# Kernel tuning notes

Hardware: AMD Instinct MI355X
Metric: run time of the kernel (lower is better)

Reference implementation:

```python
import jax, jax.numpy as jnp
import numpy as np

HIDDEN = 128
VOCAB = 100000
NUM_CLASSES = 5
N_LEAVES = 65536  # complete binary tree -> 2*N_LEAVES-1 = 131071 nodes


def setup_inputs() -> dict:
    key = jax.random.key(0)
    ks = jax.random.split(key, 24)
    H, C = HIDDEN, NUM_CLASSES

    def w(k, o, i):
        return (jax.random.normal(k, (o, i), jnp.float32) / np.sqrt(i)).astype(jnp.float32)

    def b(k, o):
        return jax.random.normal(k, (o,), jnp.float32) * 0.01

    inp = {
        "leaf_tokens": jax.random.randint(ks[0], (N_LEAVES,), 0, VOCAB, dtype=jnp.int64 if jax.config.jax_enable_x64 else jnp.int32).astype(jnp.int32),
        "node_labels": jax.random.randint(ks[1], (2 * N_LEAVES - 1,), 0, NUM_CLASSES).astype(jnp.int32),
        "embed": jax.random.uniform(ks[2], (VOCAB, H), jnp.float32, -0.5 / H, 0.5 / H),
        "W_i_w": w(ks[3], H, H), "W_i_b": b(ks[4], H),
        "W_o_w": w(ks[5], H, H), "W_o_b": b(ks[6], H),
        "W_u_w": w(ks[7], H, H), "W_u_b": b(ks[8], H),
        "U_i_w": w(ks[9], H, 2 * H), "U_i_b": b(ks[10], H),
        "U_o_w": w(ks[11], H, 2 * H), "U_o_b": b(ks[12], H),
        "U_u_w": w(ks[13], H, 2 * H), "U_u_b": b(ks[14], H),
        "F1_w": w(ks[15], H, H), "F1_b": b(ks[16], H),
        "F2_w": w(ks[17], H, H), "F2_b": b(ks[18], H),
        "out_w": w(ks[19], C, H), "out_b": b(ks[20], C),
    }
    return inp


def reference(leaf_tokens, node_labels, embed,
              W_i_w, W_i_b, W_o_w, W_o_b, W_u_w, W_u_b,
              U_i_w, U_i_b, U_o_w, U_o_b, U_u_w, U_u_b,
              F1_w, F1_b, F2_w, F2_b, out_w, out_b):
    def aff(x, wgt, bias):
        return x @ wgt.T + bias

    # ---- leaves: x = embed[token]; c = sigmoid(W_i x) * tanh(W_u x) ----
    x = embed[leaf_tokens]                          # [L, H]
    i = jax.nn.sigmoid(aff(x, W_i_w, W_i_b))
    o = jax.nn.sigmoid(aff(x, W_o_w, W_o_b))
    u = jnp.tanh(aff(x, W_u_w, W_u_b))
    c = i * u
    h = o * jnp.tanh(c)
    outs = [aff(h, out_w, out_b)]                   # dropout is identity at eval

    # ---- internal levels, bottom-up, all same-depth nodes batched ----
    n_levels = int(np.log2(N_LEAVES))
    for _ in range(n_levels):
        hl, hr = h[0::2], h[1::2]                   # [n/2, H] each
        cl, cr = c[0::2], c[1::2]
        xc = jnp.concatenate([hl, hr], axis=1)      # [n/2, 2H]
        i = jax.nn.sigmoid(aff(xc, U_i_w, U_i_b))
        o = jax.nn.sigmoid(aff(xc, U_o_w, U_o_b))
        u = jnp.tanh(aff(xc, U_u_w, U_u_b))
        f1 = jax.nn.sigmoid(aff(hl, F1_w, F1_b))
        f2 = jax.nn.sigmoid(aff(hr, F2_w, F2_b))
        c = i * u + f1 * cl + f2 * cr
        h = o * jnp.tanh(c)
        outs.append(aff(h, out_w, out_b))

    outputs = jnp.concatenate(outs, axis=0)         # [2L-1, num_classes]
    return outputs, node_labels
```

## Files before the change

### kernel.cpp

```cpp
#include <hip/hip_runtime.h>
#include <hip/hip_bf16.h>
#include <math.h>

#define H    128
#define NC   5
#define LPI  264
#define LPL  136
#define HPAD 136
#define CBP  132

typedef unsigned short ushort_t;
using frag_ab = __attribute__((ext_vector_type(8))) short;
using frag_cd = __attribute__((ext_vector_type(4))) float;

__device__ __forceinline__ float fsig(float x) { return 1.0f / (1.0f + __expf(-x)); }
__device__ __forceinline__ float ftanh_(float x) {
    float e = __expf(-2.0f * fabsf(x));
    float t = (1.0f - e) / (1.0f + e);
    return copysignf(t, x);
}
__device__ __forceinline__ ushort_t f2bf(float f) {
    __hip_bfloat16 b = __float2bfloat16(f);
    return *reinterpret_cast<ushort_t*>(&b);
}

__global__ __launch_bounds__(256) void prep_weights(
    const float* __restrict__ Ui, const float* __restrict__ Uo, const float* __restrict__ Uu,
    const float* __restrict__ F1, const float* __restrict__ F2,
    const float* __restrict__ Wi, const float* __restrict__ Wo, const float* __restrict__ Wu,
    const float* __restrict__ Wout,
    ushort_t* __restrict__ Wf, ushort_t* __restrict__ Wlf, ushort_t* __restrict__ Woutf)
{
    int e = blockIdx.x * 256 + threadIdx.x;
    if (e < 131072) {
        int kc = e >> 12, rem = e & 4095;
        int n = rem >> 3, j7 = rem & 7;
        int k = kc * 8 + j7;
        int g = n >> 7, jc = n & 127;
        float v;
        if (g == 0)      v = Ui[jc * 256 + k];
        else if (g == 1) v = Uo[jc * 256 + k];
        else if (g == 2) v = Uu[jc * 256 + k];
        else             v = (k < 128) ? F1[jc * 128 + k] : F2[jc * 128 + k - 128];
        Wf[e] = f2bf(v);
    } else if (e < 180224) {
        int e2 = e - 131072;
        int kc = e2 / 3072, rem = e2 % 3072;
        int n = rem >> 3, j7 = rem & 7;
        int k = kc * 8 + j7;
        int g = n >> 7, jc = n & 127;
        float v = (g == 0) ? Wi[jc * 128 + k] : (g == 1) ? Wo[jc * 128 + k] : Wu[jc * 128 + k];
        Wlf[e2] = f2bf(v);
    } else {
        int e3 = e - 180224;
        int kcq = e3 >> 7, rem = e3 & 127;
        int col = rem >> 3, j7 = rem & 7;
        int k = kcq * 8 + j7;
        float v = (col < NC) ? Wout[col * H + k] : 0.0f;
        Woutf[e3] = f2bf(v);
    }
}

__global__ __launch_bounds__(512) void leaf_l1_mfma(
    const int* __restrict__ tokens, const float* __restrict__ embed,
    const ushort_t* __restrict__ Wlf, const ushort_t* __restrict__ Wf,
    const ushort_t* __restrict__ Woutf,
    const float* __restrict__ bi, const float* __restrict__ bo, const float* __restrict__ bu,
    const float* __restrict__ bui, const float* __restrict__ buo, const float* __restrict__ buu,
    const float* __restrict__ bf1, const float* __restrict__ bf2,
    const float* __restrict__ bout,
    const int* __restrict__ labels, float* __restrict__ lab_out,
    ushort_t* __restrict__ h1_out, float* __restrict__ c1_out,
    float* __restrict__ out_leaf, float* __restrict__ out_l1)
{
    __shared__ ushort_t xs [32 * LPL];
    __shared__ ushort_t hh [32 * HPAD];
    __shared__ float    cbL[32 * CBP];
    __shared__ ushort_t xs2[16 * LPI];
    const int tid = threadIdx.x;
    const int node_base  = blockIdx.x * 32;
    const int node1_base = blockIdx.x * 16;

    if (tid < 64) {
        int id = blockIdx.x * 64 + tid;
        if (id < 131071) lab_out[id] = (float)labels[id];
    }

    {
        int m = tid >> 4, kp = (tid & 15) * 8;
        const float* src = embed + (size_t)tokens[node_base + m] * H + kp;
        ushort_t tmp[8];
#pragma unroll
        for (int v = 0; v < 2; ++v) {
            float4 f = *(const float4*)(src + v * 4);
            tmp[v * 4 + 0] = f2bf(f.x); tmp[v * 4 + 1] = f2bf(f.y);
            tmp[v * 4 + 2] = f2bf(f.z); tmp[v * 4 + 3] = f2bf(f.w);
        }
        *(uint4*)&xs[m * LPL + kp] = *(uint4*)tmp;
    }

    const int w = tid >> 6, lane = tid & 63;
    const int mA = lane & 15, q = lane >> 4, nlane = lane & 15;

    frag_ab wb[4];
#pragma unroll
    for (int kc8 = 0; kc8 < 4; ++kc8)
        wb[kc8] = *(const frag_ab*)&Woutf[(((kc8 * 4 + q) * 16) + nlane) * 8];
    float bout_l = (nlane < NC) ? bout[nlane] : 0.0f;

    const int jt = w;
    const int j = jt * 16 + nlane;
    __syncthreads();

    frag_ab a[2][4];
#pragma unroll
    for (int t = 0; t < 2; ++t)
#pragma unroll
        for (int kc8 = 0; kc8 < 4; ++kc8)
            a[t][kc8] = *(const frag_ab*)&xs[(t * 16 + mA) * LPL + (kc8 * 4 + q) * 8];

    {
        frag_cd acc[3][2];
#pragma unroll
        for (int g = 0; g < 3; ++g)
#pragma unroll
            for (int t = 0; t < 2; ++t) acc[g][t] = (frag_cd){0.f, 0.f, 0.f, 0.f};
#pragma unroll
        for (int kc8 = 0; kc8 < 4; ++kc8) {
            int kcq = kc8 * 4 + q;
            const ushort_t* wp = &Wlf[((size_t)kcq * 384 + jt * 16 + nlane) * 8];
#pragma unroll
            for (int g = 0; g < 3; ++g) {
                frag_ab b = *(const frag_ab*)(wp + (size_t)g * H * 8);
                acc[g][0] = __builtin_amdgcn_mfma_f32_16x16x32_bf16(a[0][kc8], b, acc[g][0], 0, 0, 0);
                acc[g][1] = __builtin_amdgcn_mfma_f32_16x16x32_bf16(a[1][kc8], b, acc[g][1], 0, 0, 0);
            }
        }
        float bi_ = bi[j], bo_ = bo[j], bu_ = bu[j];
#pragma unroll
        for (int t = 0; t < 2; ++t)
#pragma unroll
            for (int r = 0; r < 4; ++r) {
                int nloc = t * 16 + q * 4 + r;
                float i_ = fsig(acc[0][t][r] + bi_);
                float o_ = fsig(acc[1][t][r] + bo_);
                float u_ = ftanh_(acc[2][t][r] + bu_);
                float c_ = i_ * u_;
                float h_ = o_ * ftanh_(c_);
                cbL[nloc * CBP + j] = c_;
                ushort_t hb = f2bf(h_);
                hh[nloc * HPAD + j] = hb;
                xs2[(nloc >> 1) * LPI + (nloc & 1) * H + j] = hb;
            }
    }
    __syncthreads();

    frag_ab a1[8];
#pragma unroll
    for (int kc8 = 0; kc8 < 8; ++kc8)
        a1[kc8] = *(const frag_ab*)&xs2[mA * LPI + (kc8 * 4 + q) * 8];

    if (w < 2) {
        frag_cd ha = (frag_cd){0.f, 0.f, 0.f, 0.f};
#pragma unroll
        for (int kc8 = 0; kc8 < 4; ++kc8) {
            frag_ab av = *(const frag_ab*)&hh[(w * 16 + mA) * HPAD + (kc8 * 4 + q) * 8];
            ha = __builtin_amdgcn_mfma_f32_16x16x32_bf16(av, wb[kc8], ha, 0, 0, 0);
        }
        if (nlane < NC) {
#pragma unroll
            for (int r = 0; r < 4; ++r)
                out_leaf[(size_t)(node_base + w * 16 + q * 4 + r) * NC + nlane] = ha[r] + bout_l;
        }
    }
    __syncthreads();

    {
        frag_cd acc[5];
#pragma unroll
        for (int g = 0; g < 5; ++g) acc[g] = (frag_cd){0.f, 0.f, 0.f, 0.f};
#pragma unroll
        for (int kc8 = 0; kc8 < 8; ++kc8) {
            int kcq = kc8 * 4 + q;
            const ushort_t* wp = &Wf[((size_t)kcq * 512 + jt * 16 + nlane) * 8];
#pragma unroll
            for (int g = 0; g < 4; ++g) {
                frag_ab b = *(const frag_ab*)(wp + (size_t)g * H * 8);
                int gi = (g < 3) ? g : (kc8 < 4 ? 3 : 4);
                acc[gi] = __builtin_amdgcn_mfma_f32_16x16x32_bf16(a1[kc8], b, acc[gi], 0, 0, 0);
            }
        }
        float bi_ = bui[j], bo_ = buo[j], bu_ = buu[j], b1_ = bf1[j], b2_ = bf2[j];
#pragma unroll
        for (int r = 0; r < 4; ++r) {
            int nloc = q * 4 + r;
            int nd = node1_base + nloc;
            float i_  = fsig(acc[0][r] + bi_);
            float o_  = fsig(acc[1][r] + bo_);
            float u_  = ftanh_(acc[2][r] + bu_);
            float f1_ = fsig(acc[3][r] + b1_);
            float f2_ = fsig(acc[4][r] + b2_);
            float cl = cbL[(2 * nloc) * CBP + j];
            float cr = cbL[(2 * nloc + 1) * CBP + j];
            float c_ = fmaf(i_, u_, fmaf(f1_, cl, f2_ * cr));
            float h_ = o_ * ftanh_(c_);
            c1_out[(size_t)nd * H + j] = c_;
            ushort_t hb = f2bf(h_);
            h1_out[(size_t)nd * H + j] = hb;
            hh[nloc * HPAD + j] = hb;
        }
    }
    __syncthreads();

    if (w == 0) {
        frag_cd ha = (frag_cd){0.f, 0.f, 0.f, 0.f};
#pragma unroll
        for (int kc8 = 0; kc8 < 4; ++kc8) {
            frag_ab av = *(const frag_ab*)&hh[mA * HPAD + (kc8 * 4 + q) * 8];
            ha = __builtin_amdgcn_mfma_f32_16x16x32_bf16(av, wb[kc8], ha, 0, 0, 0);
        }
        if (nlane < NC) {
#pragma unroll
            for (int r = 0; r < 4; ++r)
                out_l1[(size_t)(node1_base + q * 4 + r) * NC + nlane] = ha[r] + bout_l;
        }
    }
}

__global__ __launch_bounds__(512) void subtree_mfma(
    const ushort_t* __restrict__ h_prev, const float* __restrict__ c_prev,
    const ushort_t* __restrict__ Wf, const ushort_t* __restrict__ Woutf,
    const float* __restrict__ bui, const float* __restrict__ buo, const float* __restrict__ buu,
    const float* __restrict__ bf1, const float* __restrict__ bf2,
    const float* __restrict__ bout,
    ushort_t* __restrict__ h_out, float* __restrict__ c_out,
    float* __restrict__ out_base)
{
    __shared__ ushort_t xsA[32 * LPI];
    __shared__ ushort_t xsB[16 * LPI];
    __shared__ float    cbA[32 * CBP];
    __shared__ float    cbB[16 * CBP];
    __shared__ ushort_t hh [32 * HPAD];
    const int tid = threadIdx.x;
    const int NB  = gridDim.x;

    {
        int m = tid >> 4, kp = (tid & 15) * 16;
        const uint4* s = (const uint4*)(h_prev +
            ((size_t)2 * (blockIdx.x * 32 + m) + (kp >> 7)) * H + (kp & 127));
        uint4* d = (uint4*)&xsA[m * LPI + kp];
        d[0] = s[0]; d[1] = s[1];
    }

    const int w = tid >> 6, lane = tid & 63;
    const int mA = lane & 15, q = lane >> 4, nlane = lane & 15;

    frag_ab wb[4];
#pragma unroll
    for (int kc8 = 0; kc8 < 4; ++kc8)
        wb[kc8] = *(const frag_ab*)&Woutf[(((kc8 * 4 + q) * 16) + nlane) * 8];
    float bout_l = (nlane < NC) ? bout[nlane] : 0.0f;

    const int jt = w;
    const int j = jt * 16 + nlane;
    const float bi_ = bui[j], bo_ = buo[j], bu_ = buu[j], b1_ = bf1[j], b2_ = bf2[j];

    size_t out_off = 0;
    for (int lev = 0; lev < 4; ++lev) {
        const int N = 32 >> lev;
        const int ntiles = (N + 15) >> 4;
        const int gbase = blockIdx.x * N;
        ushort_t* xs_cur = (lev & 1) ? xsB : xsA;
        ushort_t* xs_nxt = (lev & 1) ? xsA : xsB;
        float*    cb_out = (lev & 1) ? cbB : cbA;
        const float* cb_in = (lev & 1) ? cbA : cbB;
        __syncthreads();

        for (int t = 0; t < ntiles; ++t) {
            frag_cd acc[5];
#pragma unroll
            for (int g = 0; g < 5; ++g) acc[g] = (frag_cd){0.f, 0.f, 0.f, 0.f};
#pragma unroll
            for (int kc8 = 0; kc8 < 8; ++kc8) {
                int kcq = kc8 * 4 + q;
                frag_ab av = *(const frag_ab*)&xs_cur[(t * 16 + mA) * LPI + kcq * 8];
                const ushort_t* wp = &Wf[((size_t)kcq * 512 + jt * 16 + nlane) * 8];
#pragma unroll
                for (int g = 0; g < 4; ++g) {
                    frag_ab b = *(const frag_ab*)(wp + (size_t)g * H * 8);
                    int gi = (g < 3) ? g : (kc8 < 4 ? 3 : 4);
                    acc[gi] = __builtin_amdgcn_mfma_f32_16x16x32_bf16(av, b, acc[gi], 0, 0, 0);
                }
            }
#pragma unroll
            for (int r = 0; r < 4; ++r) {
                int nloc = t * 16 + q * 4 + r;
                if (nloc < N) {
                    float i_  = fsig(acc[0][r] + bi_);
                    float o_  = fsig(acc[1][r] + bo_);
                    float u_  = ftanh_(acc[2][r] + bu_);
                    float f1_ = fsig(acc[3][r] + b1_);
                    float f2_ = fsig(acc[4][r] + b2_);
                    float cl, cr;
                    if (lev == 0) {
                        cl = c_prev[((size_t)2 * (gbase + nloc)) * H + j];
                        cr = c_prev[((size_t)2 * (gbase + nloc) + 1) * H + j];
                    } else {
                        cl = cb_in[(2 * nloc) * CBP + j];
                        cr = cb_in[(2 * nloc + 1) * CBP + j];
                    }
                    float c_ = fmaf(i_, u_, fmaf(f1_, cl, f2_ * cr));
                    float h_ = o_ * ftanh_(c_);
                    ushort_t hb = f2bf(h_);
                    hh[nloc * HPAD + j] = hb;
                    if (lev < 3) {
                        cb_out[nloc * CBP + j] = c_;
                        xs_nxt[(nloc >> 1) * LPI + (nloc & 1) * H + j] = hb;
                    } else {
                        c_out[(size_t)(gbase + nloc) * H + j] = c_;
                        h_out[(size_t)(gbase + nloc) * H + j] = hb;
                    }
                }
            }
        }
        __syncthreads();
        if (w < ntiles) {
            frag_cd ha = (frag_cd){0.f, 0.f, 0.f, 0.f};
#pragma unroll
            for (int kc8 = 0; kc8 < 4; ++kc8) {
                frag_ab av = *(const frag_ab*)&hh[(w * 16 + mA) * HPAD + (kc8 * 4 + q) * 8];
                ha = __builtin_amdgcn_mfma_f32_16x16x32_bf16(av, wb[kc8], ha, 0, 0, 0);
            }
            if (nlane < NC) {
#pragma unroll
                for (int r = 0; r < 4; ++r) {
                    int nd = w * 16 + q * 4 + r;
                    if (nd < N)
                        out_base[out_off + (size_t)(gbase + nd) * NC + nlane] = ha[r] + bout_l;
                }
            }
        }
        out_off += (size_t)NB * N * NC;
    }
}

__global__ __launch_bounds__(512) void tail_mfma(
    const ushort_t* __restrict__ h_prev, const float* __restrict__ c_prev,
    const ushort_t* __restrict__ Wf, const ushort_t* __restrict__ Woutf,
    const float* __restrict__ bui, const float* __restrict__ buo, const float* __restrict__ buu,
    const float* __restrict__ bf1, const float* __restrict__ bf2,
    const float* __restrict__ bout, float* __restrict__ out)
{
    __shared__ ushort_t xsA[64 * LPI];
    __shared__ ushort_t xsB[32 * LPI];
    __shared__ float    cbA[64 * H];
    __shared__ float    cbB[32 * H];
    __shared__ ushort_t hh[64 * HPAD];
    const int tid = threadIdx.x;
    const int w = tid >> 6, lane = tid & 63;
    const int mA = lane & 15, q = lane >> 4, nlane = lane & 15;

    {
        int m = tid >> 3, kp = (tid & 7) * 32;
        const uint4* s = (const uint4*)(h_prev + ((size_t)2 * m + (kp >> 7)) * H + (kp & 127));
        uint4* d = (uint4*)&xsA[m * LPI + kp];
#pragma unroll
        for (int i = 0; i < 4; ++i) d[i] = s[i];
    }

    frag_ab wb[4];
#pragma unroll
    for (int kc8 = 0; kc8 < 4; ++kc8)
        wb[kc8] = *(const frag_ab*)&Woutf[(((kc8 * 4 + q) * 16) + nlane) * 8];
    float bout_l = (nlane < NC) ? bout[nlane] : 0.0f;

    const int jt = w;
    const int j = jt * 16 + nlane;
    const float bi_ = bui[j], bo_ = buo[j], bu_ = buu[j], b1_ = bf1[j], b2_ = bf2[j];

    float* outp = out;
    for (int lev = 0; lev < 7; ++lev) {
        const int N = 64 >> lev;
        const int ntiles = (N + 15) >> 4;
        ushort_t* xs_cur = (lev & 1) ? xsB : xsA;
        ushort_t* xs_nxt = (lev & 1) ? xsA : xsB;
        float*    cb_out = (lev & 1) ? cbB : cbA;
        const float* cb_in = (lev & 1) ? cbA : cbB;
        __syncthreads();

        for (int t = 0; t < ntiles; ++t) {
            frag_cd acc[5];
#pragma unroll
            for (int g = 0; g < 5; ++g) acc[g] = (frag_cd){0.f, 0.f, 0.f, 0.f};
#pragma unroll
            for (int kc8 = 0; kc8 < 8; ++kc8) {
                int kcq = kc8 * 4 + q;
                frag_ab av = *(const frag_ab*)&xs_cur[(t * 16 + mA) * LPI + kcq * 8];
                const ushort_t* wp = &Wf[((size_t)kcq * 512 + jt * 16 + nlane) * 8];
#pragma unroll
                for (int g = 0; g < 4; ++g) {
                    frag_ab b = *(const frag_ab*)(wp + (size_t)g * H * 8);
                    int gi = (g < 3) ? g : (kc8 < 4 ? 3 : 4);
                    acc[gi] = __builtin_amdgcn_mfma_f32_16x16x32_bf16(av, b, acc[gi], 0, 0, 0);
                }
            }
#pragma unroll
            for (int r = 0; r < 4; ++r) {
                int nloc = t * 16 + q * 4 + r;
                if (nloc < N) {
                    float i_  = fsig(acc[0][r] + bi_);
                    float o_  = fsig(acc[1][r] + bo_);
                    float u_  = ftanh_(acc[2][r] + bu_);
                    float f1_ = fsig(acc[3][r] + b1_);
                    float f2_ = fsig(acc[4][r] + b2_);
                    float cl, cr;
                    if (lev == 0) {
                        cl = c_prev[((size_t)2 * nloc) * H + j];
                        cr = c_prev[((size_t)2 * nloc + 1) * H + j];
                    } else {
                        cl = cb_in[(2 * nloc) * H + j];
                        cr = cb_in[(2 * nloc + 1) * H + j];
                    }
                    float c_ = fmaf(i_, u_, fmaf(f1_, cl, f2_ * cr));
                    float h_ = o_ * ftanh_(c_);
                    cb_out[nloc * H + j] = c_;
                    ushort_t hb = f2bf(h_);
                    hh[nloc * HPAD + j] = hb;
                    xs_nxt[(nloc >> 1) * LPI + (nloc & 1) * H + j] = hb;
                }
            }
        }
        __syncthreads();
        if (w < ntiles) {
            frag_cd ha = (frag_cd){0.f, 0.f, 0.f, 0.f};
#pragma unroll
            for (int kc8 = 0; kc8 < 4; ++kc8) {
                frag_ab av = *(const frag_ab*)&hh[(w * 16 + mA) * HPAD + (kc8 * 4 + q) * 8];
                ha = __builtin_amdgcn_mfma_f32_16x16x32_bf16(av, wb[kc8], ha, 0, 0, 0);
            }
            if (nlane < NC) {
#pragma unroll
                for (int r = 0; r < 4; ++r) {
                    int nd = w * 16 + q * 4 + r;
                    if (nd < N) outp[(size_t)nd * NC + nlane] = ha[r] + bout_l;
                }
            }
        }
        outp += (size_t)N * NC;
    }
}

extern "C" void kernel_launch(void* const* d_in, const int* in_sizes, int n_in,
                              void* d_out, int out_size, void* d_ws, size_t ws_size,
                              hipStream_t stream)
{
    const int*   tokens = (const int*)d_in[0];
    const int*   labels = (const int*)d_in[1];
    const float* embed  = (const float*)d_in[2];
    const float* Wi = (const float*)d_in[3];  const float* bi  = (const float*)d_in[4];
    const float* Wo = (const float*)d_in[5];  const float* bo  = (const float*)d_in[6];
    const float* Wu = (const float*)d_in[7];  const float* bu  = (const float*)d_in[8];
    const float* Ui = (const float*)d_in[9];  const float* bui = (const float*)d_in[10];
    const float* Uo = (const float*)d_in[11]; const float* buo = (const float*)d_in[12];
    const float* Uu = (const float*)d_in[13]; const float* buu = (const float*)d_in[14];
    const float* F1 = (const float*)d_in[15]; const float* bf1 = (const float*)d_in[16];
    const float* F2 = (const float*)d_in[17]; const float* bf2 = (const float*)d_in[18];
    const float* Wout = (const float*)d_in[19]; const float* bout = (const float*)d_in[20];
    float* out = (float*)d_out;

    const int NL = 65536;
    char* base = (char*)d_ws;
    ushort_t* Wf    = (ushort_t*)(base);
    ushort_t* Wlf   = (ushort_t*)(base + 327680);
    ushort_t* Woutf = (ushort_t*)(base + 425984);
    ushort_t* hA    = (ushort_t*)(base + 430080);
    ushort_t* hB    = (ushort_t*)(base + 17207296);
    float*    cA    = (float*)   (base + 25595904);
    float*    cB    = (float*)   (base + 59150336);

    prep_weights<<<712, 256, 0, stream>>>(Ui, Uo, Uu, F1, F2, Wi, Wo, Wu, Wout,
                                          Wf, Wlf, Woutf);

    const size_t totalN = 2 * (size_t)NL - 1;
    float* lab_out = out + totalN * NC;

    leaf_l1_mfma<<<NL / 32, 512, 0, stream>>>(
        tokens, embed, Wlf, Wf, Woutf, bi, bo, bu, bui, buo, buu, bf1, bf2,
        bout, labels, lab_out, hB, cB, out, out + (size_t)NL * NC);

    size_t off = (size_t)(NL + NL / 2) * NC;

    subtree_mfma<<<512, 512, 0, stream>>>(
        hB, cB, Wf, Woutf, bui, buo, buu, bf1, bf2, bout, hA, cA, out + off);
    off += (size_t)(16384 + 8192 + 4096 + 2048) * NC;

    subtree_mfma<<<32, 512, 0, stream>>>(
        hA, cA, Wf, Woutf, bui, buo, buu, bf1, bf2, bout, hB, cB, out + off);
    off += (size_t)(1024 + 512 + 256 + 128) * NC;

    tail_mfma<<<1, 512, 0, stream>>>(hB, cB, Wf, Woutf, bui, buo, buu, bf1, bf2,
                                     bout, out + off);
}
```

Measured before the change: 252.3 us.

## Fuse tree levels 2 and 3 into leaf kernel and rebalance subtree launches

```diff
diff --git a/kernel.cpp b/kernel.cpp
--- a/kernel.cpp
+++ b/kernel.cpp
@@ -61,7 +61,7 @@
     }
 }
 
-__global__ __launch_bounds__(512) void leaf_l1_mfma(
+__global__ __launch_bounds__(512) void leaf_l3_mfma(
     const int* __restrict__ tokens, const float* __restrict__ embed,
     const ushort_t* __restrict__ Wlf, const ushort_t* __restrict__ Wf,
     const ushort_t* __restrict__ Woutf,
@@ -70,25 +70,28 @@
     const float* __restrict__ bf1, const float* __restrict__ bf2,
     const float* __restrict__ bout,
     const int* __restrict__ labels, float* __restrict__ lab_out,
-    ushort_t* __restrict__ h1_out, float* __restrict__ c1_out,
-    float* __restrict__ out_leaf, float* __restrict__ out_l1)
+    ushort_t* __restrict__ h3_out, float* __restrict__ c3_out,
+    float* __restrict__ out)
 {
     __shared__ ushort_t xs [32 * LPL];
     __shared__ ushort_t hh [32 * HPAD];
     __shared__ float    cbL[32 * CBP];
     __shared__ ushort_t xs2[16 * LPI];
+    __shared__ float    cb1[16 * CBP];
+    __shared__ ushort_t xs3[16 * LPI];
+    __shared__ float    cb2[8  * CBP];
+    __shared__ ushort_t xs4[16 * LPI];
     const int tid = threadIdx.x;
-    const int node_base  = blockIdx.x * 32;
-    const int node1_base = blockIdx.x * 16;
+    const int nb  = blockIdx.x;
 
     if (tid < 64) {
-        int id = blockIdx.x * 64 + tid;
+        int id = nb * 64 + tid;
         if (id < 131071) lab_out[id] = (float)labels[id];
     }
 
     {
         int m = tid >> 4, kp = (tid & 15) * 8;
-        const float* src = embed + (size_t)tokens[node_base + m] * H + kp;
+        const float* src = embed + (size_t)tokens[nb * 32 + m] * H + kp;
         ushort_t tmp[8];
 #pragma unroll
         for (int v = 0; v < 2; ++v) {
@@ -110,6 +113,8 @@
 
     const int jt = w;
     const int j = jt * 16 + nlane;
+    const float bui_ = bui[j], buo_ = buo[j], buu_ = buu[j];
+    const float bf1_ = bf1[j], bf2_ = bf2[j];
     __syncthreads();
 
     frag_ab a[2][4];
@@ -170,7 +175,7 @@
         if (nlane < NC) {
 #pragma unroll
             for (int r = 0; r < 4; ++r)
-                out_leaf[(size_t)(node_base + w * 16 + q * 4 + r) * NC + nlane] = ha[r] + bout_l;
+                out[(size_t)(nb * 32 + w * 16 + q * 4 + r) * NC + nlane] = ha[r] + bout_l;
         }
     }
     __syncthreads();
@@ -190,27 +195,30 @@
                 acc[gi] = __builtin_amdgcn_mfma_f32_16x16x32_bf16(a1[kc8], b, acc[gi], 0, 0, 0);
             }
         }
-        float bi_ = bui[j], bo_ = buo[j], bu_ = buu[j], b1_ = bf1[j], b2_ = bf2[j];
 #pragma unroll
         for (int r = 0; r < 4; ++r) {
             int nloc = q * 4 + r;
-            int nd = node1_base + nloc;
-            float i_  = fsig(acc[0][r] + bi_);
-            float o_  = fsig(acc[1][r] + bo_);
-            float u_  = ftanh_(acc[2][r] + bu_);
-            float f1_ = fsig(acc[3][r] + b1_);
-            float f2_ = fsig(acc[4][r] + b2_);
+            float i_  = fsig(acc[0][r] + bui_);
+            float o_  = fsig(acc[1][r] + buo_);
+            float u_  = ftanh_(acc[2][r] + buu_);
+            float f1_ = fsig(acc[3][r] + bf1_);
+            float f2_ = fsig(acc[4][r] + bf2_);
             float cl = cbL[(2 * nloc) * CBP + j];
             float cr = cbL[(2 * nloc + 1) * CBP + j];
             float c_ = fmaf(i_, u_, fmaf(f1_, cl, f2_ * cr));
             float h_ = o_ * ftanh_(c_);
-            c1_out[(size_t)nd * H + j] = c_;
+            cb1[nloc * CBP + j] = c_;
             ushort_t hb = f2bf(h_);
-            h1_out[(size_t)nd * H + j] = hb;
             hh[nloc * HPAD + j] = hb;
-        }
-    }
-    __syncthreads();
+            xs3[(nloc >> 1) * LPI + (nloc & 1) * H + j] = hb;
+        }
+    }
+    __syncthreads();
+
+    frag_ab a2[8];
+#pragma unroll
+    for (int kc8 = 0; kc8 < 8; ++kc8)
+        a2[kc8] = *(const frag_ab*)&xs3[mA * LPI + (kc8 * 4 + q) * 8];
 
     if (w == 0) {
         frag_cd ha = (frag_cd){0.f, 0.f, 0.f, 0.f};
@@ -222,7 +230,122 @@
         if (nlane < NC) {
 #pragma unroll
             for (int r = 0; r < 4; ++r)
-                out_l1[(size_t)(node1_base + q * 4 + r) * NC + nlane] = ha[r] + bout_l;
+                out[(size_t)65536 * NC + (size_t)(nb * 16 + q * 4 + r) * NC + nlane] = ha[r] + bout_l;
+        }
+    }
+    __syncthreads();
+
+    {
+        frag_cd acc[5];
+#pragma unroll
+        for (int g = 0; g < 5; ++g) acc[g] = (frag_cd){0.f, 0.f, 0.f, 0.f};
+#pragma unroll
+        for (int kc8 = 0; kc8 < 8; ++kc8) {
+            int kcq = kc8 * 4 + q;
+            const ushort_t* wp = &Wf[((size_t)kcq * 512 + jt * 16 + nlane) * 8];
+#pragma unroll
+            for (int g = 0; g < 4; ++g) {
+                frag_ab b = *(const frag_ab*)(wp + (size_t)g * H * 8);
+                int gi = (g < 3) ? g : (kc8 < 4 ? 3 : 4);
+                acc[gi] = __builtin_amdgcn_mfma_f32_16x16x32_bf16(a2[kc8], b, acc[gi], 0, 0, 0);
+            }
+        }
+#pragma unroll
+        for (int r = 0; r < 4; ++r) {
+            int nloc = q * 4 + r;
+            if (nloc < 8) {
+                float i_  = fsig(acc[0][r] + bui_);
+                float o_  = fsig(acc[1][r] + buo_);
+                float u_  = ftanh_(acc[2][r] + buu_);
+                float f1_ = fsig(acc[3][r] + bf1_);
+                float f2_ = fsig(acc[4][r] + bf2_);
+                float cl = cb1[(2 * nloc) * CBP + j];
+                float cr = cb1[(2 * nloc + 1) * CBP + j];
+                float c_ = fmaf(i_, u_, fmaf(f1_, cl, f2_ * cr));
+                float h_ = o_ * ftanh_(c_);
+                cb2[nloc * CBP + j] = c_;
+                ushort_t hb = f2bf(h_);
+                hh[nloc * HPAD + j] = hb;
+                xs4[(nloc >> 1) * LPI + (nloc & 1) * H + j] = hb;
+            }
+        }
+    }
+    __syncthreads();
+
+    frag_ab a3[8];
+#pragma unroll
+    for (int kc8 = 0; kc8 < 8; ++kc8)
+        a3[kc8] = *(const frag_ab*)&xs4[mA * LPI + (kc8 * 4 + q) * 8];
+
+    if (w == 0) {
+        frag_cd ha = (frag_cd){0.f, 0.f, 0.f, 0.f};
+#pragma unroll
+        for (int kc8 = 0; kc8 < 4; ++kc8) {
+            frag_ab av = *(const frag_ab*)&hh[mA * HPAD + (kc8 * 4 + q) * 8];
+            ha = __builtin_amdgcn_mfma_f32_16x16x32_bf16(av, wb[kc8], ha, 0, 0, 0);
+        }
+        if (nlane < NC) {
+#pragma unroll
+            for (int r = 0; r < 4; ++r) {
+                int nd = q * 4 + r;
+                if (nd < 8)
+                    out[(size_t)98304 * NC + (size_t)(nb * 8 + nd) * NC + nlane] = ha[r] + bout_l;
+            }
+        }
+    }
+    __syncthreads();
+
+    {
+        frag_cd acc[5];
+#pragma unroll
+        for (int g = 0; g < 5; ++g) acc[g] = (frag_cd){0.f, 0.f, 0.f, 0.f};
+#pragma unroll
+        for (int kc8 = 0; kc8 < 8; ++kc8) {
+            int kcq = kc8 * 4 + q;
+            const ushort_t* wp = &Wf[((size_t)kcq * 512 + jt * 16 + nlane) * 8];
+#pragma unroll
+            for (int g = 0; g < 4; ++g) {
+                frag_ab b = *(const frag_ab*)(wp + (size_t)g * H * 8);
+                int gi = (g < 3) ? g : (kc8 < 4 ? 3 : 4);
+                acc[gi] = __builtin_amdgcn_mfma_f32_16x16x32_bf16(a3[kc8], b, acc[gi], 0, 0, 0);
+            }
+        }
+#pragma unroll
+        for (int r = 0; r < 4; ++r) {
+            int nloc = q * 4 + r;
+            if (nloc < 4) {
+                float i_  = fsig(acc[0][r] + bui_);
+                float o_  = fsig(acc[1][r] + buo_);
+                float u_  = ftanh_(acc[2][r] + buu_);
+                float f1_ = fsig(acc[3][r] + bf1_);
+                float f2_ = fsig(acc[4][r] + bf2_);
+                float cl = cb2[(2 * nloc) * CBP + j];
+                float cr = cb2[(2 * nloc + 1) * CBP + j];
+                float c_ = fmaf(i_, u_, fmaf(f1_, cl, f2_ * cr));
+                float h_ = o_ * ftanh_(c_);
+                c3_out[(size_t)(nb * 4 + nloc) * H + j] = c_;
+                ushort_t hb = f2bf(h_);
+                h3_out[(size_t)(nb * 4 + nloc) * H + j] = hb;
+                hh[nloc * HPAD + j] = hb;
+            }
+        }
+    }
+    __syncthreads();
+
+    if (w == 0) {
+        frag_cd ha = (frag_cd){0.f, 0.f, 0.f, 0.f};
+#pragma unroll
+        for (int kc8 = 0; kc8 < 4; ++kc8) {
+            frag_ab av = *(const frag_ab*)&hh[mA * HPAD + (kc8 * 4 + q) * 8];
+            ha = __builtin_amdgcn_mfma_f32_16x16x32_bf16(av, wb[kc8], ha, 0, 0, 0);
+        }
+        if (nlane < NC) {
+#pragma unroll
+            for (int r = 0; r < 4; ++r) {
+                int nd = q * 4 + r;
+                if (nd < 4)
+                    out[(size_t)114688 * NC + (size_t)(nb * 4 + nd) * NC + nlane] = ha[r] + bout_l;
+            }
         }
     }
 }
@@ -266,6 +389,7 @@
     const float bi_ = bui[j], bo_ = buo[j], bu_ = buu[j], b1_ = bf1[j], b2_ = bf2[j];
 
     size_t out_off = 0;
+#pragma unroll 1
     for (int lev = 0; lev < 4; ++lev) {
         const int N = 32 >> lev;
         const int ntiles = (N + 15) >> 4;
@@ -351,21 +475,19 @@
     const float* __restrict__ bf1, const float* __restrict__ bf2,
     const float* __restrict__ bout, float* __restrict__ out)
 {
-    __shared__ ushort_t xsA[64 * LPI];
-    __shared__ ushort_t xsB[32 * LPI];
-    __shared__ float    cbA[64 * H];
-    __shared__ float    cbB[32 * H];
-    __shared__ ushort_t hh[64 * HPAD];
+    __shared__ ushort_t xsA[16 * LPI];
+    __shared__ ushort_t xsB[16 * LPI];
+    __shared__ float    cbA[16 * H];
+    __shared__ float    cbB[8 * H];
+    __shared__ ushort_t hh[16 * HPAD];
     const int tid = threadIdx.x;
     const int w = tid >> 6, lane = tid & 63;
     const int mA = lane & 15, q = lane >> 4, nlane = lane & 15;
 
     {
-        int m = tid >> 3, kp = (tid & 7) * 32;
+        int m = tid >> 5, kp = (tid & 31) * 8;
         const uint4* s = (const uint4*)(h_prev + ((size_t)2 * m + (kp >> 7)) * H + (kp & 127));
-        uint4* d = (uint4*)&xsA[m * LPI + kp];
-#pragma unroll
-        for (int i = 0; i < 4; ++i) d[i] = s[i];
+        *(uint4*)&xsA[m * LPI + kp] = s[0];
     }
 
     frag_ab wb[4];
@@ -379,23 +501,23 @@
     const float bi_ = bui[j], bo_ = buo[j], bu_ = buu[j], b1_ = bf1[j], b2_ = bf2[j];
 
     float* outp = out;
-    for (int lev = 0; lev < 7; ++lev) {
-        const int N = 64 >> lev;
-        const int ntiles = (N + 15) >> 4;
+#pragma unroll 1
+    for (int lev = 0; lev < 5; ++lev) {
+        const int N = 16 >> lev;
         ushort_t* xs_cur = (lev & 1) ? xsB : xsA;
         ushort_t* xs_nxt = (lev & 1) ? xsA : xsB;
         float*    cb_out = (lev & 1) ? cbB : cbA;
         const float* cb_in = (lev & 1) ? cbA : cbB;
         __syncthreads();
 
-        for (int t = 0; t < ntiles; ++t) {
+        {
             frag_cd acc[5];
 #pragma unroll
             for (int g = 0; g < 5; ++g) acc[g] = (frag_cd){0.f, 0.f, 0.f, 0.f};
 #pragma unroll
             for (int kc8 = 0; kc8 < 8; ++kc8) {
                 int kcq = kc8 * 4 + q;
-                frag_ab av = *(const frag_ab*)&xs_cur[(t * 16 + mA) * LPI + kcq * 8];
+                frag_ab av = *(const frag_ab*)&xs_cur[mA * LPI + kcq * 8];
                 const ushort_t* wp = &Wf[((size_t)kcq * 512 + jt * 16 + nlane) * 8];
 #pragma unroll
                 for (int g = 0; g < 4; ++g) {
@@ -406,7 +528,7 @@
             }
 #pragma unroll
             for (int r = 0; r < 4; ++r) {
-                int nloc = t * 16 + q * 4 + r;
+                int nloc = q * 4 + r;
                 if (nloc < N) {
                     float i_  = fsig(acc[0][r] + bi_);
                     float o_  = fsig(acc[1][r] + bo_);
@@ -431,17 +553,17 @@
             }
         }
         __syncthreads();
-        if (w < ntiles) {
+        if (w == 0) {
             frag_cd ha = (frag_cd){0.f, 0.f, 0.f, 0.f};
 #pragma unroll
             for (int kc8 = 0; kc8 < 4; ++kc8) {
-                frag_ab av = *(const frag_ab*)&hh[(w * 16 + mA) * HPAD + (kc8 * 4 + q) * 8];
+                frag_ab av = *(const frag_ab*)&hh[mA * HPAD + (kc8 * 4 + q) * 8];
                 ha = __builtin_amdgcn_mfma_f32_16x16x32_bf16(av, wb[kc8], ha, 0, 0, 0);
             }
             if (nlane < NC) {
 #pragma unroll
                 for (int r = 0; r < 4; ++r) {
-                    int nd = w * 16 + q * 4 + r;
+                    int nd = q * 4 + r;
                     if (nd < N) outp[(size_t)nd * NC + nlane] = ha[r] + bout_l;
                 }
             }
@@ -484,20 +606,18 @@
     const size_t totalN = 2 * (size_t)NL - 1;
     float* lab_out = out + totalN * NC;
 
-    leaf_l1_mfma<<<NL / 32, 512, 0, stream>>>(
+    leaf_l3_mfma<<<NL / 32, 512, 0, stream>>>(
         tokens, embed, Wlf, Wf, Woutf, bi, bo, bu, bui, buo, buu, bf1, bf2,
-        bout, labels, lab_out, hB, cB, out, out + (size_t)NL * NC);
-
-    size_t off = (size_t)(NL + NL / 2) * NC;
-
-    subtree_mfma<<<512, 512, 0, stream>>>(
-        hB, cB, Wf, Woutf, bui, buo, buu, bf1, bf2, bout, hA, cA, out + off);
-    off += (size_t)(16384 + 8192 + 4096 + 2048) * NC;
-
-    subtree_mfma<<<32, 512, 0, stream>>>(
-        hA, cA, Wf, Woutf, bui, buo, buu, bf1, bf2, bout, hB, cB, out + off);
-    off += (size_t)(1024 + 512 + 256 + 128) * NC;
+        bout, labels, lab_out, hB, cB, out);
+
+    subtree_mfma<<<128, 512, 0, stream>>>(
+        hB, cB, Wf, Woutf, bui, buo, buu, bf1, bf2, bout, hA, cA,
+        out + (size_t)122880 * NC);
+
+    subtree_mfma<<<8, 512, 0, stream>>>(
+        hA, cA, Wf, Woutf, bui, buo, buu, bf1, bf2, bout, hB, cB,
+        out + (size_t)130560 * NC);
 
     tail_mfma<<<1, 512, 0, stream>>>(hB, cB, Wf, Woutf, bui, buo, buu, bf1, bf2,
-                                     bout, out + off);
+                                     bout, out + (size_t)131040 * NC);
 }
```

After: 289.5 us. 1.15x slower.
